# Kernel optimization log

Measured on AMD Instinct MI355X. Metric: run time of the kernel, lower is better.

## Reference

```python
import jax, jax.numpy as jnp
import numpy as np

PARTITIONS = 8
TWO_PI = 2.0 * np.pi
EPS_COUNT = 0.0001  # added to bin counts to avoid div-by-zero


def setup_inputs() -> dict:
    key = jax.random.key(0)
    k1, k2, k3, k4 = jax.random.split(key, 4)
    B, N, T = 16384, 128, 8
    trajs = jax.random.normal(k1, (B, T, 2), dtype=jnp.float32)
    nei_trajs = jax.random.normal(k2, (B, N, T, 2), dtype=jnp.float32)
    # mark last 32 neighbors as invalid (all-zero trajectories -> masked out)
    nei_trajs = nei_trajs.at[:, N - 32:].set(0.0)
    # TrajEncoding: Dense(dim=3 -> output_units=128) + ReLU
    W_ce = jax.random.normal(k3, (3, 128), dtype=jnp.float32) * (1.0 / np.sqrt(3.0))
    b_ce = jnp.zeros((128,), dtype=jnp.float32)
    return {"trajs": trajs, "nei_trajs": nei_trajs, "W_ce": W_ce, "b_ce": b_ce}


def reference(trajs, nei_trajs, W_ce, b_ce):
    # trajs: [B, T, 2]; nei_trajs: [B, N, T, 2]
    nei_vector = nei_trajs[..., -1, :] - nei_trajs[..., 0, :]      # [B, N, 2]
    nei_pos = nei_trajs[..., -1, :]                                 # [B, N, 2]

    # factors (use_velocity, use_distance, use_direction; rel_velocity=False)
    f_velocity = jnp.linalg.norm(nei_vector, axis=-1)               # [B, N]
    f_distance = jnp.linalg.norm(nei_pos, axis=-1)                  # [B, N]
    f_direction = jnp.arctan2(nei_pos[..., 0], nei_pos[..., 1]) % TWO_PI  # [B, N]

    angle_idx = (f_direction / (TWO_PI / PARTITIONS)).astype(jnp.int32)   # [B, N]
    nei_mask = (jnp.sum(nei_trajs, axis=(-1, -2)) != 0).astype(jnp.int32)  # [B, N]
    angle_idx = angle_idx * nei_mask + (-1) * (1 - nei_mask)

    # one-hot over partitions replaces the python loop: [B, N, P]
    onehot = (angle_idx[..., None] == jnp.arange(PARTITIONS, dtype=jnp.int32)).astype(jnp.float32)
    n = jnp.sum(onehot, axis=1) + EPS_COUNT                         # [B, P]

    feats = jnp.stack([f_velocity, f_distance, f_direction], axis=-1)  # [B, N, 3]
    sums = jnp.einsum('bnf,bnp->bpf', feats, onehot)                # [B, P, 3]
    social_circle = sums / n[..., None]                             # [B, P, 3]

    f_sc = jax.nn.relu(social_circle @ W_ce + b_ce)                 # [B, P, 128]
    return f_sc, social_circle
```

## Files before the change

kernel.cpp:

```cpp
#include <hip/hip_runtime.h>
#include <math.h>

#define NPART 8
#define NN    128
#define TT    8

__global__ __launch_bounds__(128) void sc_kernel(
    const float* __restrict__ nei,
    const float* __restrict__ W,
    const float* __restrict__ bce,
    float* __restrict__ fsc,
    float* __restrict__ scout,
    int Btot)
{
    const int b = blockIdx.x;
    if (b >= Btot) return;
    const int tid = threadIdx.x;

    __shared__ float s_sum[NPART * 3];
    __shared__ float s_cnt[NPART];
    __shared__ float s_sc[NPART * 3];

    if (tid < NPART * 3) s_sum[tid] = 0.0f;
    if (tid < NPART)     s_cnt[tid] = 0.0f;
    __syncthreads();

    const float4* p4 = reinterpret_cast<const float4*>(nei) + ((size_t)b * NN + tid) * 4;
    float4 a = p4[0];
    float4 c = p4[1];
    float4 d = p4[2];
    float4 e = p4[3];

    float total = (((a.x + a.y) + (a.z + a.w)) + ((c.x + c.y) + (c.z + c.w)))
                + (((d.x + d.y) + (d.z + d.w)) + ((e.x + e.y) + (e.z + e.w)));

    float px = e.z, py = e.w;
    float vx = px - a.x, vy = py - a.y;
    float fvel  = sqrtf(vx * vx + vy * vy);
    float fdist = sqrtf(px * px + py * py);

    float fdir = atan2f(px, py);
    if (fdir < 0.0f) fdir += 6.2831853071795864769f;

    const float STEP = (float)(6.283185307179586 / 8.0);
    int idx = (int)(fdir / STEP);

    if (total != 0.0f && idx >= 0 && idx < NPART) {
        atomicAdd(&s_sum[idx * 3 + 0], fvel);
        atomicAdd(&s_sum[idx * 3 + 1], fdist);
        atomicAdd(&s_sum[idx * 3 + 2], fdir);
        atomicAdd(&s_cnt[idx], 1.0f);
    }
    __syncthreads();

    if (tid < NPART * 3) {
        float v = s_sum[tid] / (s_cnt[tid / 3] + 0.0001f);
        s_sc[tid] = v;
        scout[(size_t)b * (NPART * 3) + tid] = v;
    }
    __syncthreads();

    float w0 = W[tid], w1 = W[NN + tid], w2 = W[2 * NN + tid];
    float bb = bce[tid];
    float* o = fsc + (size_t)b * NPART * NN;
    #pragma unroll
    for (int p = 0; p < NPART; ++p) {
        float acc = bb;
        acc = fmaf(s_sc[p * 3 + 0], w0, acc);
        acc = fmaf(s_sc[p * 3 + 1], w1, acc);
        acc = fmaf(s_sc[p * 3 + 2], w2, acc);
        o[p * NN + tid] = fmaxf(acc, 0.0f);
    }
}

extern "C" void kernel_launch(void* const* d_in, const int* in_sizes, int n_in,
                              void* d_out, int out_size, void* d_ws, size_t ws_size,
                              hipStream_t stream) {
    const float* nei = (const float*)d_in[1];
    const float* W   = (const float*)d_in[2];
    const float* bce = (const float*)d_in[3];

    const int Btot = in_sizes[1] / (NN * TT * 2);

    float* fsc   = (float*)d_out;
    float* scout = fsc + (size_t)Btot * NPART * NN;

    sc_kernel<<<Btot, 128, 0, stream>>>(nei, W, bce, fsc, scout, Btot);
}
```

Measured before the change: 47.08 us.

## Stage neighbor trajectories through LDS with coalesced async loads and XOR swizzle

Each block now copies its 8 KB neighbor slice straight into LDS using global_load_lds, so every load instruction reads contiguous memory instead of each thread reading its own 64-byte row with a stride. An XOR swizzle on the LDS layout is meant to keep the per-thread float4 reads free of bank conflicts. The W and bias loads are moved ahead of the wait so they overlap with the async copy. This adds 8 KB of LDS per block, which may lower occupancy, plus some index arithmetic.

```diff
diff --git a/kernel.cpp b/kernel.cpp
--- a/kernel.cpp
+++ b/kernel.cpp
@@ -3,7 +3,7 @@
 
 #define NPART 8
 #define NN    128
-#define TT    8
+#define B_UNITS 512
 
 __global__ __launch_bounds__(128) void sc_kernel(
     const float* __restrict__ nei,
@@ -13,23 +13,48 @@
     float* __restrict__ scout,
     int Btot)
 {
-    const int b = blockIdx.x;
+    const int b    = blockIdx.x;
     if (b >= Btot) return;
-    const int tid = threadIdx.x;
+    const int tid  = threadIdx.x;
+    const int lane = tid & 63;
+    const int wv   = tid >> 6;
 
-    __shared__ float s_sum[NPART * 3];
-    __shared__ float s_cnt[NPART];
-    __shared__ float s_sc[NPART * 3];
+    __shared__ float4 st[B_UNITS];
+    __shared__ float  s_sum[NPART * 3];
+    __shared__ float  s_cnt[NPART];
+    __shared__ float  s_sc[NPART * 3];
+
+    float w0 = W[tid], w1 = W[NN + tid], w2 = W[2 * NN + tid];
+    float bb = bce[tid];
+
+    const float4* src = reinterpret_cast<const float4*>(nei) + (size_t)b * B_UNITS;
+
+    #pragma unroll
+    for (int k = 0; k < 4; ++k) {
+        int u  = k * 128 + wv * 64 + lane;
+        int b2 = ((u >> 2) ^ (u >> 4)) & 1;
+        int b1 = ((u >> 1) ^ (u >> 3)) & 1;
+        int b0 = (u ^ b2) & 1;
+        int j  = (u & ~7) | (b2 << 2) | (b1 << 1) | b0;
+        __builtin_amdgcn_global_load_lds(
+            (const __attribute__((address_space(1))) void*)(src + j),
+            (__attribute__((address_space(3))) void*)(st + k * 128 + wv * 64),
+            16, 0, 0);
+    }
 
     if (tid < NPART * 3) s_sum[tid] = 0.0f;
     if (tid < NPART)     s_cnt[tid] = 0.0f;
+    asm volatile("s_waitcnt vmcnt(0)");
     __syncthreads();
 
-    const float4* p4 = reinterpret_cast<const float4*>(nei) + ((size_t)b * NN + tid) * 4;
-    float4 a = p4[0];
-    float4 c = p4[1];
-    float4 d = p4[2];
-    float4 e = p4[3];
+    float4 a, c, d, e;
+    {
+        int m = tid & 7;
+        a = st[(tid * 4 + 0) ^ m];
+        c = st[(tid * 4 + 1) ^ m];
+        d = st[(tid * 4 + 2) ^ m];
+        e = st[(tid * 4 + 3) ^ m];
+    }
 
     float total = (((a.x + a.y) + (a.z + a.w)) + ((c.x + c.y) + (c.z + c.w)))
                 + (((d.x + d.y) + (d.z + d.w)) + ((e.x + e.y) + (e.z + e.w)));
@@ -60,8 +85,6 @@
     }
     __syncthreads();
 
-    float w0 = W[tid], w1 = W[NN + tid], w2 = W[2 * NN + tid];
-    float bb = bce[tid];
     float* o = fsc + (size_t)b * NPART * NN;
     #pragma unroll
     for (int p = 0; p < NPART; ++p) {
@@ -80,7 +103,7 @@
     const float* W   = (const float*)d_in[2];
     const float* bce = (const float*)d_in[3];
 
-    const int Btot = in_sizes[1] / (NN * TT * 2);
+    const int Btot = in_sizes[1] / (NN * 8 * 2);
 
     float* fsc   = (float*)d_out;
     float* scout = fsc + (size_t)Btot * NPART * NN;
```

Result: slower. 51.23 us (+8.8%).

## Process one batch row per wavefront with two neighbors per lane

Applied to the files above, without the earlier changes.

Each 64-lane wavefront now handles one batch element, with four wavefronts per 256-thread block. Each lane processes two neighbors, and block-wide __syncthreads are replaced by wave barriers over per-wave shared accumulators. The output projection is written as float2 stores, two channels per lane. The aim is to cut block-level synchronization and launch granularity for a memory-bound kernel, at the cost of more registers per lane and fewer concurrent loads per element.

```diff
diff --git a/kernel.cpp b/kernel.cpp
--- a/kernel.cpp
+++ b/kernel.cpp
@@ -3,9 +3,9 @@
 
 #define NPART 8
 #define NN    128
-#define TT    8
+#define WPB   4
 
-__global__ __launch_bounds__(128) void sc_kernel(
+__global__ __launch_bounds__(256) void sc_kernel(
     const float* __restrict__ nei,
     const float* __restrict__ W,
     const float* __restrict__ bce,
@@ -13,63 +13,85 @@
     float* __restrict__ scout,
     int Btot)
 {
-    const int b = blockIdx.x;
+    const int tid  = threadIdx.x;
+    const int lane = tid & 63;
+    const int wv   = tid >> 6;
+    const int b    = blockIdx.x * WPB + wv;
     if (b >= Btot) return;
-    const int tid = threadIdx.x;
 
-    __shared__ float s_sum[NPART * 3];
-    __shared__ float s_cnt[NPART];
-    __shared__ float s_sc[NPART * 3];
+    __shared__ float s_sum[WPB][NPART * 3];
+    __shared__ float s_cnt[WPB][NPART];
+    __shared__ float s_sc[WPB][NPART * 3];
 
-    if (tid < NPART * 3) s_sum[tid] = 0.0f;
-    if (tid < NPART)     s_cnt[tid] = 0.0f;
-    __syncthreads();
+    const float4* src = reinterpret_cast<const float4*>(nei) + (size_t)b * (NN * 4);
+    float4 a0 = src[lane * 4 + 0];
+    float4 c0 = src[lane * 4 + 1];
+    float4 d0 = src[lane * 4 + 2];
+    float4 e0 = src[lane * 4 + 3];
+    float4 a1 = src[256 + lane * 4 + 0];
+    float4 c1 = src[256 + lane * 4 + 1];
+    float4 d1 = src[256 + lane * 4 + 2];
+    float4 e1 = src[256 + lane * 4 + 3];
 
-    const float4* p4 = reinterpret_cast<const float4*>(nei) + ((size_t)b * NN + tid) * 4;
-    float4 a = p4[0];
-    float4 c = p4[1];
-    float4 d = p4[2];
-    float4 e = p4[3];
+    const int c0i = 2 * lane, c1i = 2 * lane + 1;
+    float2 wr0 = *reinterpret_cast<const float2*>(W + 0 * NN + c0i);
+    float2 wr1 = *reinterpret_cast<const float2*>(W + 1 * NN + c0i);
+    float2 wr2 = *reinterpret_cast<const float2*>(W + 2 * NN + c0i);
+    float2 bb  = *reinterpret_cast<const float2*>(bce + c0i);
 
-    float total = (((a.x + a.y) + (a.z + a.w)) + ((c.x + c.y) + (c.z + c.w)))
-                + (((d.x + d.y) + (d.z + d.w)) + ((e.x + e.y) + (e.z + e.w)));
+    if (lane < NPART * 3) s_sum[wv][lane] = 0.0f;
+    if (lane < NPART)     s_cnt[wv][lane] = 0.0f;
+    __builtin_amdgcn_wave_barrier();
 
-    float px = e.z, py = e.w;
-    float vx = px - a.x, vy = py - a.y;
-    float fvel  = sqrtf(vx * vx + vy * vy);
-    float fdist = sqrtf(px * px + py * py);
+    const float TWOPI = 6.2831853071795864769f;
+    const float STEP  = (float)(6.283185307179586 / 8.0);
 
-    float fdir = atan2f(px, py);
-    if (fdir < 0.0f) fdir += 6.2831853071795864769f;
+    #pragma unroll
+    for (int h = 0; h < 2; ++h) {
+        float4 a = h ? a1 : a0;
+        float4 c = h ? c1 : c0;
+        float4 d = h ? d1 : d0;
+        float4 e = h ? e1 : e0;
 
-    const float STEP = (float)(6.283185307179586 / 8.0);
-    int idx = (int)(fdir / STEP);
+        float total = (((a.x + a.y) + (a.z + a.w)) + ((c.x + c.y) + (c.z + c.w)))
+                    + (((d.x + d.y) + (d.z + d.w)) + ((e.x + e.y) + (e.z + e.w)));
 
-    if (total != 0.0f && idx >= 0 && idx < NPART) {
-        atomicAdd(&s_sum[idx * 3 + 0], fvel);
-        atomicAdd(&s_sum[idx * 3 + 1], fdist);
-        atomicAdd(&s_sum[idx * 3 + 2], fdir);
-        atomicAdd(&s_cnt[idx], 1.0f);
+        float px = e.z, py = e.w;
+        float vx = px - a.x, vy = py - a.y;
+        float fvel  = sqrtf(vx * vx + vy * vy);
+        float fdist = sqrtf(px * px + py * py);
+
+        float fdir = atan2f(px, py);
+        if (fdir < 0.0f) fdir += TWOPI;
+
+        int idx = (int)(fdir / STEP);
+
+        if (total != 0.0f && idx >= 0 && idx < NPART) {
+            atomicAdd(&s_sum[wv][idx * 3 + 0], fvel);
+            atomicAdd(&s_sum[wv][idx * 3 + 1], fdist);
+            atomicAdd(&s_sum[wv][idx * 3 + 2], fdir);
+            atomicAdd(&s_cnt[wv][idx], 1.0f);
+        }
     }
-    __syncthreads();
+    __builtin_amdgcn_wave_barrier();
 
-    if (tid < NPART * 3) {
-        float v = s_sum[tid] / (s_cnt[tid / 3] + 0.0001f);
-        s_sc[tid] = v;
-        scout[(size_t)b * (NPART * 3) + tid] = v;
+    if (lane < NPART * 3) {
+        float v = s_sum[wv][lane] / (s_cnt[wv][lane / 3] + 0.0001f);
+        s_sc[wv][lane] = v;
+        scout[(size_t)b * (NPART * 3) + lane] = v;
     }
-    __syncthreads();
+    __builtin_amdgcn_wave_barrier();
 
-    float w0 = W[tid], w1 = W[NN + tid], w2 = W[2 * NN + tid];
-    float bb = bce[tid];
     float* o = fsc + (size_t)b * NPART * NN;
     #pragma unroll
     for (int p = 0; p < NPART; ++p) {
-        float acc = bb;
-        acc = fmaf(s_sc[p * 3 + 0], w0, acc);
-        acc = fmaf(s_sc[p * 3 + 1], w1, acc);
-        acc = fmaf(s_sc[p * 3 + 2], w2, acc);
-        o[p * NN + tid] = fmaxf(acc, 0.0f);
+        float sv = s_sc[wv][p * 3 + 0];
+        float sd = s_sc[wv][p * 3 + 1];
+        float sr = s_sc[wv][p * 3 + 2];
+        float2 acc;
+        acc.x = fmaxf(fmaf(sv, wr0.x, fmaf(sd, wr1.x, fmaf(sr, wr2.x, bb.x))), 0.0f);
+        acc.y = fmaxf(fmaf(sv, wr0.y, fmaf(sd, wr1.y, fmaf(sr, wr2.y, bb.y))), 0.0f);
+        *reinterpret_cast<float2*>(o + p * NN + c0i) = acc;
     }
 }
 
@@ -80,10 +102,11 @@
     const float* W   = (const float*)d_in[2];
     const float* bce = (const float*)d_in[3];
 
-    const int Btot = in_sizes[1] / (NN * TT * 2);
+    const int Btot = in_sizes[1] / (NN * 8 * 2);
 
     float* fsc   = (float*)d_out;
     float* scout = fsc + (size_t)Btot * NPART * NN;
 
-    sc_kernel<<<Btot, 128, 0, stream>>>(nei, W, bce, fsc, scout, Btot);
+    const int nblk = (Btot + WPB - 1) / WPB;
+    sc_kernel<<<nblk, 256, 0, stream>>>(nei, W, bce, fsc, scout, Btot);
 }
```

Measured after the change: 43.90 us. 1.07x faster.
